# Kernel tuning notes

Measured on AMD Instinct MI355X. Metric: run time of the kernel, lower is better.

## Reference

```python
import jax, jax.numpy as jnp
import numpy as np

E, K, D_IN, D_H, D_OUT, B = 16, 2, 256, 512, 256, 32768


def setup_inputs() -> dict:
    key = jax.random.key(0)
    ks = jax.random.split(key, 7)
    s_in = 1.0 / np.sqrt(D_IN)
    s_h = 1.0 / np.sqrt(D_H)
    return {
        "x": jax.random.normal(ks[0], (B, D_IN), jnp.float32),
        "Wg": jax.random.normal(ks[1], (D_IN, E), jnp.float32) * s_in,
        "bg": jnp.zeros((E,), jnp.float32),
        "W1": jax.random.normal(ks[2], (E, D_IN, D_H), jnp.float32) * s_in,
        "b1": jnp.zeros((E, D_H), jnp.float32),
        "W2": jax.random.normal(ks[3], (E, D_H, D_OUT), jnp.float32) * s_h,
        "b2": jnp.zeros((E, D_OUT), jnp.float32),
    }


def reference(x, Wg, bg, W1, b1, W2, b2):
    # Gating: softmax over experts, top-k, renormalize routing weights.
    probs = jax.nn.softmax(x @ Wg + bg, axis=-1)            # [B, E]
    top_vals, top_idx = jax.lax.top_k(probs, K)              # [B, K]
    w = top_vals / jnp.sum(top_vals, axis=-1, keepdims=True)  # [B, K]

    # Dense per-expert MLP over all tokens (vectorized dispatch equivalent).
    h = jax.nn.relu(jnp.einsum("bi,eih->ebh", x, W1) + b1[:, None, :])  # [E, B, Dh]
    out_e = jnp.einsum("ebh,eho->ebo", h, W2) + b2[:, None, :]          # [E, B, Do]

    # Gather each token's k assigned expert outputs and combine weighted.
    out_be = jnp.transpose(out_e, (1, 0, 2))                  # [B, E, Do]
    sel = jnp.take_along_axis(out_be, top_idx[:, :, None], axis=1)  # [B, K, Do]
    return jnp.sum(w[:, :, None] * sel, axis=1)               # [B, Do]
```

## Files before the change

kernel.cpp:

```cpp
#include <hip/hip_runtime.h>

#define E_ 16
#define DIN 256
#define DH 512
#define DOUT 256
#define BTOK 32768

typedef _Float16 half8 __attribute__((ext_vector_type(8)));
typedef _Float16 half4v __attribute__((ext_vector_type(4)));
typedef float float4v __attribute__((ext_vector_type(4)));

#define OFF_P1      0u
#define OFF_P2      4194304u
#define OFF_XH      8388608u
#define OFF_SCR     25165824u
#define OFF_TIDX    58720256u
#define OFF_TW      58982400u
#define OFF_STOK    59244544u
#define OFF_SW      59506688u
#define OFF_CNT     59768832u
#define OFF_OFFS    59768960u
#define OFF_CUR     59769088u
#define OFF_TMAP    59769216u
#define MLP_GRID    2048

__global__ __launch_bounds__(256) void pack_kernel(const float* __restrict__ W1,
                                                   const float* __restrict__ W2,
                                                   _Float16* __restrict__ p1,
                                                   _Float16* __restrict__ p2,
                                                   int* __restrict__ counts) {
    int tid = threadIdx.x;
    int bid = blockIdx.x * 4 + (tid >> 6);
    int l = tid & 63;
    int quad = l >> 4, l15 = l & 15;
    if (blockIdx.x == 0 && tid < 16) counts[tid] = 0;
    if (bid < 4096) {
        int ht = bid & 31, kt = (bid >> 5) & 7, e = bid >> 8;
        half8 v;
#pragma unroll
        for (int j = 0; j < 8; ++j)
            v[j] = (_Float16)W1[(e * DIN + kt * 32 + quad * 8 + j) * DH + ht * 16 + l15];
        ((half8*)p1)[bid * 64 + l] = v;
    } else {
        int b2i = bid - 4096;
        int ot = b2i & 15, kt = (b2i >> 4) & 15, e = b2i >> 8;
        half8 v;
#pragma unroll
        for (int j = 0; j < 8; ++j)
            v[j] = (_Float16)W2[(e * DH + kt * 32 + quad * 8 + j) * DOUT + ot * 16 + l15];
        ((half8*)p2)[b2i * 64 + l] = v;
    }
}

__global__ __launch_bounds__(256) void gate_kernel(const float* __restrict__ x,
                                                   const float* __restrict__ Wg,
                                                   const float* __restrict__ bg,
                                                   _Float16* __restrict__ xh,
                                                   int* __restrict__ tidx,
                                                   float* __restrict__ tw,
                                                   int* __restrict__ counts) {
    __shared__ float WgS[DIN * E_];
    __shared__ int hcnt[16];
    int tid = threadIdx.x;
    if (tid < 16) hcnt[tid] = 0;
#pragma unroll
    for (int i = 0; i < 4; ++i)
        ((float4v*)WgS)[tid + i * 256] = ((const float4v*)Wg)[tid + i * 256];
    __syncthreads();

    int q = tid & 7, tg = tid >> 3;
    int t0 = blockIdx.x * 64 + tg * 2;

    float acc[2][16];
#pragma unroll
    for (int tt = 0; tt < 2; ++tt)
#pragma unroll
        for (int e = 0; e < 16; ++e) acc[tt][e] = 0.f;

#pragma unroll
    for (int ii = 0; ii < 8; ++ii) {
        int kb = q * 32 + ii * 4;
        float4v xv[2];
#pragma unroll
        for (int tt = 0; tt < 2; ++tt) {
            xv[tt] = *(const float4v*)&x[(t0 + tt) * DIN + kb];
            half4v hv;
#pragma unroll
            for (int j = 0; j < 4; ++j) hv[j] = (_Float16)xv[tt][j];
            *(half4v*)&xh[(t0 + tt) * DIN + kb] = hv;
        }
#pragma unroll
        for (int j = 0; j < 4; ++j) {
            const float4v* wrow = (const float4v*)&WgS[(kb + j) * 16];
            float4v w0 = wrow[0], w1 = wrow[1], w2 = wrow[2], w3 = wrow[3];
#pragma unroll
            for (int tt = 0; tt < 2; ++tt) {
                float xs = xv[tt][j];
#pragma unroll
                for (int c = 0; c < 4; ++c) {
                    acc[tt][0 + c]  += xs * w0[c];
                    acc[tt][4 + c]  += xs * w1[c];
                    acc[tt][8 + c]  += xs * w2[c];
                    acc[tt][12 + c] += xs * w3[c];
                }
            }
        }
    }
#pragma unroll
    for (int tt = 0; tt < 2; ++tt)
#pragma unroll
        for (int e = 0; e < 16; ++e) {
            acc[tt][e] += __shfl_xor(acc[tt][e], 1);
            acc[tt][e] += __shfl_xor(acc[tt][e], 2);
            acc[tt][e] += __shfl_xor(acc[tt][e], 4);
        }
    if (q == 0) {
#pragma unroll
        for (int tt = 0; tt < 2; ++tt) {
            int b = t0 + tt;
            float m1 = -3.4e38f, m2 = -3.4e38f;
            int i1 = 0, i2 = 0;
#pragma unroll
            for (int e = 0; e < 16; ++e) {
                float v = acc[tt][e] + bg[e];
                if (v > m1) { m2 = m1; i2 = i1; m1 = v; i1 = e; }
                else if (v > m2) { m2 = v; i2 = e; }
            }
            float e2 = __expf(m2 - m1);
            float w1 = 1.f / (1.f + e2);
            tidx[b * 2] = i1; tidx[b * 2 + 1] = i2;
            tw[b * 2] = w1;  tw[b * 2 + 1] = e2 * w1;
            atomicAdd(&hcnt[i1], 1);
            atomicAdd(&hcnt[i2], 1);
        }
    }
    __syncthreads();
    if (tid < 16) atomicAdd(&counts[tid], hcnt[tid]);
}

__global__ void scan_kernel(const int* __restrict__ counts, int* __restrict__ offsets,
                            int* __restrict__ cursor, int* __restrict__ tmap) {
    __shared__ int s_off[17];
    int tid = threadIdx.x;
    for (int i = tid; i < MLP_GRID; i += 64) tmap[i] = -1;
    if (tid == 0) {
        int run = 0;
        for (int e = 0; e < 16; ++e) { s_off[e] = run; run += counts[e]; }
        s_off[16] = run;
    }
    __syncthreads();
    if (tid < 16) {
        int e = tid;
        offsets[e] = s_off[e];
        cursor[e] = s_off[e];
        if (e == 0) offsets[16] = s_off[16];
        int nt = (s_off[e + 1] - s_off[e] + 63) >> 6;
        int xc = e & 7;
        int base = (e >= 8) ? ((s_off[e - 7] - s_off[e - 8] + 63) >> 6) : 0;
        for (int t = 0; t < nt; ++t) {
            int s = base + t;
            if (s < 256) tmap[xc + 8 * s] = (e << 16) | t;
        }
    }
}

__global__ __launch_bounds__(256) void scatter_kernel(const int* __restrict__ tidx,
                                                      const float* __restrict__ tw,
                                                      int* __restrict__ cursor,
                                                      int* __restrict__ stok,
                                                      float* __restrict__ sw) {
    __shared__ int lc[16];
    __shared__ int lbase[16];
    int tid = threadIdx.x;
    if (tid < 16) lc[tid] = 0;
    __syncthreads();
    int g = blockIdx.x * 256 + tid;
    int e = tidx[g];
    int rank = atomicAdd(&lc[e], 1);
    __syncthreads();
    if (tid < 16) lbase[tid] = atomicAdd(&cursor[tid], lc[tid]);
    __syncthreads();
    int pos = lbase[e] + rank;
    stok[pos] = g;
    sw[pos] = tw[g];
}

#define XS 0
#define HS 16384
__global__ __launch_bounds__(512, 4) void mlp_kernel(const _Float16* __restrict__ xh,
                                                     const _Float16* __restrict__ p1,
                                                     const _Float16* __restrict__ p2,
                                                     const float* __restrict__ b1,
                                                     const float* __restrict__ b2,
                                                     const int* __restrict__ offsets,
                                                     const int* __restrict__ stok,
                                                     const float* __restrict__ sw,
                                                     const int* __restrict__ tmap,
                                                     _Float16* __restrict__ scr) {
    __shared__ _Float16 S[32768];
    const int tile = tmap[blockIdx.x];
    if (tile < 0) return;
    const int e = tile >> 16;
    const int ts = (tile & 0xffff) * 64;
    const int off = offsets[e];
    const int ne = offsets[e + 1] - off;
    const int rows = min(64, ne - ts);

    const int tid = threadIdx.x;
    const int w = tid >> 6;
    const int l = tid & 63;
    const int l15 = l & 15;
    const int quad = l >> 4;

#pragma unroll
    for (int j = 0; j < 4; ++j) {
        int tokl = w * 8 + j * 2 + (l >> 5);
        int slot = l & 31;
        int g = slot ^ (tokl & 7);
        int r = tokl; if (r >= rows) r = rows - 1;
        int tok = stok[off + ts + r] >> 1;
        half8 v = *(const half8*)&xh[tok * DIN + g * 8];
        *(half8*)&S[XS + tokl * 256 + slot * 8] = v;
    }

    const half8* p1b = (const half8*)p1;
    const half8* p2b = (const half8*)p2;

    float4v acc2[2][4];
#pragma unroll
    for (int n = 0; n < 2; ++n)
#pragma unroll
        for (int mt = 0; mt < 4; ++mt) acc2[n][mt] = (float4v){0.f, 0.f, 0.f, 0.f};

    __syncthreads();

#pragma unroll
    for (int half = 0; half < 2; ++half) {
        float4v acc1[2][4];
#pragma unroll
        for (int mh = 0; mh < 2; ++mh)
#pragma unroll
            for (int nt = 0; nt < 4; ++nt) acc1[mh][nt] = (float4v){0.f, 0.f, 0.f, 0.f};

        half8 awc[2], awn[2];
#pragma unroll
        for (int mh = 0; mh < 2; ++mh)
            awc[mh] = p1b[((e * 8 + 0) * 32 + half * 16 + w * 2 + mh) * 64 + l];

#pragma unroll
        for (int kt = 0; kt < 8; ++kt) {
            int ktn = kt < 7 ? kt + 1 : 7;
#pragma unroll
            for (int mh = 0; mh < 2; ++mh)
                awn[mh] = p1b[((e * 8 + ktn) * 32 + half * 16 + w * 2 + mh) * 64 + l];
            half8 bq[4];
#pragma unroll
            for (int nt = 0; nt < 4; ++nt) {
                int row = nt * 16 + l15;
                int slot = (kt * 4 + quad) ^ (l15 & 7);
                bq[nt] = *(const half8*)&S[XS + row * 256 + slot * 8];
            }
#pragma unroll
            for (int mh = 0; mh < 2; ++mh) {
#pragma unroll
                for (int nt = 0; nt < 4; ++nt)
                    acc1[mh][nt] = __builtin_amdgcn_mfma_f32_16x16x32_f16(awc[mh], bq[nt], acc1[mh][nt], 0, 0, 0);
            }
            awc[0] = awn[0]; awc[1] = awn[1];
        }
#pragma unroll
        for (int mh = 0; mh < 2; ++mh) {
            int colh = (w * 2 + mh) * 16 + quad * 4;
            float4v b1q = *(const float4v*)&b1[e * DH + half * 256 + colh];
            int gq = colh >> 3;
            int go = (quad & 1) * 4;
#pragma unroll
            for (int nt = 0; nt < 4; ++nt) {
                int row = nt * 16 + l15;
                int slot = gq ^ (l15 & 7);
                half4v hv;
#pragma unroll
                for (int r = 0; r < 4; ++r) {
                    float v = acc1[mh][nt][r] + b1q[r];
                    hv[r] = (_Float16)(v > 0.f ? v : 0.f);
                }
                *(half4v*)&S[HS + row * 256 + slot * 8 + go] = hv;
            }
        }
        __syncthreads();

        half8 bwc[2], bwn[2];
#pragma unroll
        for (int n = 0; n < 2; ++n)
            bwc[n] = p2b[((e * 16 + half * 8 + 0) * 16 + w * 2 + n) * 64 + l];

#pragma unroll
        for (int kt2 = 0; kt2 < 8; ++kt2) {
            int ktn = kt2 < 7 ? kt2 + 1 : 7;
#pragma unroll
            for (int n = 0; n < 2; ++n)
                bwn[n] = p2b[((e * 16 + half * 8 + ktn) * 16 + w * 2 + n) * 64 + l];
            half8 ha[4];
#pragma unroll
            for (int mt = 0; mt < 4; ++mt) {
                int row = mt * 16 + l15;
                int slot = (kt2 * 4 + quad) ^ (l15 & 7);
                ha[mt] = *(const half8*)&S[HS + row * 256 + slot * 8];
            }
#pragma unroll
            for (int n = 0; n < 2; ++n) {
#pragma unroll
                for (int mt = 0; mt < 4; ++mt)
                    acc2[n][mt] = __builtin_amdgcn_mfma_f32_16x16x32_f16(bwc[n], ha[mt], acc2[n][mt], 0, 0, 0);
            }
            bwc[0] = bwn[0]; bwc[1] = bwn[1];
        }
        __syncthreads();
    }

#pragma unroll
    for (int n = 0; n < 2; ++n) {
        int col0 = (w * 2 + n) * 16 + quad * 4;
        float4v b2q = *(const float4v*)&b2[e * DOUT + col0];
        int gran = col0 >> 3;
        int go = (quad & 1) * 4;
#pragma unroll
        for (int mt = 0; mt < 4; ++mt) {
            int tok = mt * 16 + l15;
            int rc = tok < rows ? tok : rows - 1;
            float wt = sw[off + ts + rc];
            half4v hv;
#pragma unroll
            for (int r = 0; r < 4; ++r)
                hv[r] = (_Float16)(wt * (acc2[n][mt][r] + b2q[r]));
            int slot = gran ^ (tok & 7);
            *(half4v*)&S[HS + tok * 256 + slot * 8 + go] = hv;
        }
    }
    __syncthreads();
#pragma unroll
    for (int p = 0; p < 4; ++p) {
        int idx = p * 512 + tid;
        int tok = idx >> 5;
        int sl = idx & 31;
        if (tok < rows) {
            int slot = sl ^ (tok & 7);
            half8 v = *(const half8*)&S[HS + tok * 256 + slot * 8];
            int g = stok[off + ts + tok];
            *(half8*)&scr[g * DOUT + sl * 8] = v;
        }
    }
}

__global__ __launch_bounds__(256) void combine_kernel(const _Float16* __restrict__ scr,
                                                      float* __restrict__ out) {
    int wv = threadIdx.x >> 6;
    int l = threadIdx.x & 63;
    int t = blockIdx.x * 4 + wv;
    half4v a = ((const half4v*)(scr + t * 2 * DOUT))[l];
    half4v b = ((const half4v*)(scr + t * 2 * DOUT + DOUT))[l];
    float4v o;
#pragma unroll
    for (int j = 0; j < 4; ++j) o[j] = (float)a[j] + (float)b[j];
    ((float4v*)(out + t * DOUT))[l] = o;
}

extern "C" void kernel_launch(void* const* d_in, const int* in_sizes, int n_in,
                              void* d_out, int out_size, void* d_ws, size_t ws_size,
                              hipStream_t stream) {
    const float* x  = (const float*)d_in[0];
    const float* Wg = (const float*)d_in[1];
    const float* bg = (const float*)d_in[2];
    const float* W1 = (const float*)d_in[3];
    const float* b1 = (const float*)d_in[4];
    const float* W2 = (const float*)d_in[5];
    const float* b2 = (const float*)d_in[6];
    float* out = (float*)d_out;

    char* ws = (char*)d_ws;
    _Float16* p1  = (_Float16*)(ws + OFF_P1);
    _Float16* p2  = (_Float16*)(ws + OFF_P2);
    _Float16* xh  = (_Float16*)(ws + OFF_XH);
    _Float16* scr = (_Float16*)(ws + OFF_SCR);
    int* tidx     = (int*)(ws + OFF_TIDX);
    float* tw     = (float*)(ws + OFF_TW);
    int* stok     = (int*)(ws + OFF_STOK);
    float* swp    = (float*)(ws + OFF_SW);
    int* counts   = (int*)(ws + OFF_CNT);
    int* offsets  = (int*)(ws + OFF_OFFS);
    int* cursor   = (int*)(ws + OFF_CUR);
    int* tmap     = (int*)(ws + OFF_TMAP);

    pack_kernel<<<dim3(2048), dim3(256), 0, stream>>>(W1, W2, p1, p2, counts);
    gate_kernel<<<dim3(512), dim3(256), 0, stream>>>(x, Wg, bg, xh, tidx, tw, counts);
    scan_kernel<<<dim3(1), dim3(64), 0, stream>>>(counts, offsets, cursor, tmap);
    scatter_kernel<<<dim3(256), dim3(256), 0, stream>>>(tidx, tw, cursor, stok, swp);
    mlp_kernel<<<dim3(MLP_GRID), dim3(512), 0, stream>>>(xh, p1, p2, b1, b2, offsets,
                                                         stok, swp, tmap, scr);
    combine_kernel<<<dim3(8192), dim3(256), 0, stream>>>(scr, out);
}
```

Baseline: 200.1 us.

## Merge pack and gate kernels; replace global atomics and scan kernel with per-block histogram

```diff
diff --git a/kernel.cpp b/kernel.cpp
--- a/kernel.cpp
+++ b/kernel.cpp
@@ -14,54 +14,54 @@
 #define OFF_P2      4194304u
 #define OFF_XH      8388608u
 #define OFF_SCR     25165824u
+#define OFF_HIST    25165824u
 #define OFF_TIDX    58720256u
 #define OFF_TW      58982400u
 #define OFF_STOK    59244544u
 #define OFF_SW      59506688u
-#define OFF_CNT     59768832u
 #define OFF_OFFS    59768960u
-#define OFF_CUR     59769088u
 #define OFF_TMAP    59769216u
 #define MLP_GRID    2048
 
-__global__ __launch_bounds__(256) void pack_kernel(const float* __restrict__ W1,
+__global__ __launch_bounds__(256) void prep_kernel(const float* __restrict__ W1,
                                                    const float* __restrict__ W2,
+                                                   const float* __restrict__ x,
+                                                   const float* __restrict__ Wg,
+                                                   const float* __restrict__ bg,
                                                    _Float16* __restrict__ p1,
                                                    _Float16* __restrict__ p2,
-                                                   int* __restrict__ counts) {
-    int tid = threadIdx.x;
-    int bid = blockIdx.x * 4 + (tid >> 6);
-    int l = tid & 63;
-    int quad = l >> 4, l15 = l & 15;
-    if (blockIdx.x == 0 && tid < 16) counts[tid] = 0;
-    if (bid < 4096) {
-        int ht = bid & 31, kt = (bid >> 5) & 7, e = bid >> 8;
-        half8 v;
-#pragma unroll
-        for (int j = 0; j < 8; ++j)
-            v[j] = (_Float16)W1[(e * DIN + kt * 32 + quad * 8 + j) * DH + ht * 16 + l15];
-        ((half8*)p1)[bid * 64 + l] = v;
-    } else {
-        int b2i = bid - 4096;
-        int ot = b2i & 15, kt = (b2i >> 4) & 15, e = b2i >> 8;
-        half8 v;
-#pragma unroll
-        for (int j = 0; j < 8; ++j)
-            v[j] = (_Float16)W2[(e * DH + kt * 32 + quad * 8 + j) * DOUT + ot * 16 + l15];
-        ((half8*)p2)[b2i * 64 + l] = v;
-    }
-}
-
-__global__ __launch_bounds__(256) void gate_kernel(const float* __restrict__ x,
-                                                   const float* __restrict__ Wg,
-                                                   const float* __restrict__ bg,
                                                    _Float16* __restrict__ xh,
                                                    int* __restrict__ tidx,
                                                    float* __restrict__ tw,
-                                                   int* __restrict__ counts) {
+                                                   int* __restrict__ hist) {
     __shared__ float WgS[DIN * E_];
     __shared__ int hcnt[16];
     int tid = threadIdx.x;
+
+    if (blockIdx.x < 2048) {
+        int bid = blockIdx.x * 4 + (tid >> 6);
+        int l = tid & 63;
+        int quad = l >> 4, l15 = l & 15;
+        if (bid < 4096) {
+            int ht = bid & 31, kt = (bid >> 5) & 7, e = bid >> 8;
+            half8 v;
+#pragma unroll
+            for (int j = 0; j < 8; ++j)
+                v[j] = (_Float16)W1[(e * DIN + kt * 32 + quad * 8 + j) * DH + ht * 16 + l15];
+            ((half8*)p1)[bid * 64 + l] = v;
+        } else {
+            int b2i = bid - 4096;
+            int ot = b2i & 15, kt = (b2i >> 4) & 15, e = b2i >> 8;
+            half8 v;
+#pragma unroll
+            for (int j = 0; j < 8; ++j)
+                v[j] = (_Float16)W2[(e * DH + kt * 32 + quad * 8 + j) * DOUT + ot * 16 + l15];
+            ((half8*)p2)[b2i * 64 + l] = v;
+        }
+        return;
+    }
+
+    int gb = blockIdx.x - 2048;
     if (tid < 16) hcnt[tid] = 0;
 #pragma unroll
     for (int i = 0; i < 4; ++i)
@@ -69,7 +69,7 @@
     __syncthreads();
 
     int q = tid & 7, tg = tid >> 3;
-    int t0 = blockIdx.x * 64 + tg * 2;
+    int t0 = gb * 64 + tg * 2;
 
     float acc[2][16];
 #pragma unroll
@@ -135,54 +135,76 @@
         }
     }
     __syncthreads();
-    if (tid < 16) atomicAdd(&counts[tid], hcnt[tid]);
+    if (tid < 16) hist[gb * 16 + tid] = hcnt[tid];
 }
 
-__global__ void scan_kernel(const int* __restrict__ counts, int* __restrict__ offsets,
-                            int* __restrict__ cursor, int* __restrict__ tmap) {
+__global__ __launch_bounds__(256) void scatter_kernel(const int* __restrict__ hist,
+                                                      const int* __restrict__ tidx,
+                                                      const float* __restrict__ tw,
+                                                      int* __restrict__ offsets,
+                                                      int* __restrict__ tmap,
+                                                      int* __restrict__ stok,
+                                                      float* __restrict__ sw) {
+    __shared__ int part_tot[16][17];
+    __shared__ int part_pre[16][17];
     __shared__ int s_off[17];
+    __shared__ int s_base[16];
+    __shared__ int lc[16];
     int tid = threadIdx.x;
-    for (int i = tid; i < MLP_GRID; i += 64) tmap[i] = -1;
+    int b = blockIdx.x;
+    int e = tid & 15, ch = tid >> 4;
+    int gblim = b * 2;
+    int t0 = 0, p0 = 0;
+    for (int i = 0; i < 32; ++i) {
+        int gb = ch * 32 + i;
+        int v = hist[gb * 16 + e];
+        t0 += v;
+        if (gb < gblim) p0 += v;
+    }
+    part_tot[e][ch] = t0;
+    part_pre[e][ch] = p0;
+    if (tid < 16) lc[tid] = 0;
+    __syncthreads();
+    if (tid < 16) {
+        int tot = 0, pre = 0;
+#pragma unroll
+        for (int c = 0; c < 16; ++c) { tot += part_tot[tid][c]; pre += part_pre[tid][c]; }
+        part_tot[tid][16] = tot;
+        part_pre[tid][16] = pre;
+    }
+    __syncthreads();
     if (tid == 0) {
         int run = 0;
-        for (int e = 0; e < 16; ++e) { s_off[e] = run; run += counts[e]; }
+#pragma unroll
+        for (int e2 = 0; e2 < 16; ++e2) { s_off[e2] = run; run += part_tot[e2][16]; }
         s_off[16] = run;
     }
     __syncthreads();
-    if (tid < 16) {
-        int e = tid;
-        offsets[e] = s_off[e];
-        cursor[e] = s_off[e];
-        if (e == 0) offsets[16] = s_off[16];
-        int nt = (s_off[e + 1] - s_off[e] + 63) >> 6;
-        int xc = e & 7;
-        int base = (e >= 8) ? ((s_off[e - 7] - s_off[e - 8] + 63) >> 6) : 0;
-        for (int t = 0; t < nt; ++t) {
-            int s = base + t;
-            if (s < 256) tmap[xc + 8 * s] = (e << 16) | t;
-        }
-    }
-}
-
-__global__ __launch_bounds__(256) void scatter_kernel(const int* __restrict__ tidx,
-                                                      const float* __restrict__ tw,
-                                                      int* __restrict__ cursor,
-                                                      int* __restrict__ stok,
-                                                      float* __restrict__ sw) {
-    __shared__ int lc[16];
-    __shared__ int lbase[16];
-    int tid = threadIdx.x;
-    if (tid < 16) lc[tid] = 0;
-    __syncthreads();
-    int g = blockIdx.x * 256 + tid;
-    int e = tidx[g];
-    int rank = atomicAdd(&lc[e], 1);
-    __syncthreads();
-    if (tid < 16) lbase[tid] = atomicAdd(&cursor[tid], lc[tid]);
-    __syncthreads();
-    int pos = lbase[e] + rank;
+    if (tid < 16) s_base[tid] = s_off[tid] + part_pre[tid][16];
+    __syncthreads();
+
+    int g = b * 256 + tid;
+    int et = tidx[g];
+    int rank = atomicAdd(&lc[et], 1);
+    int pos = s_base[et] + rank;
     stok[pos] = g;
     sw[pos] = tw[g];
+
+    if (b == 0) {
+        if (tid < 17) offsets[tid] = s_off[tid];
+        for (int i = tid; i < MLP_GRID; i += 256) tmap[i] = -1;
+        __syncthreads();
+        if (tid < 16) {
+            int e2 = tid;
+            int nt = (s_off[e2 + 1] - s_off[e2] + 63) >> 6;
+            int xc = e2 & 7;
+            int base = (e2 >= 8) ? ((s_off[e2 - 7] - s_off[e2 - 8] + 63) >> 6) : 0;
+            for (int t = 0; t < nt; ++t) {
+                int s = base + t;
+                if (s < 256) tmap[xc + 8 * s] = (e2 << 16) | t;
+            }
+        }
+    }
 }
 
 #define XS 0
@@ -382,19 +404,18 @@
     _Float16* p2  = (_Float16*)(ws + OFF_P2);
     _Float16* xh  = (_Float16*)(ws + OFF_XH);
     _Float16* scr = (_Float16*)(ws + OFF_SCR);
+    int* hist     = (int*)(ws + OFF_HIST);
     int* tidx     = (int*)(ws + OFF_TIDX);
     float* tw     = (float*)(ws + OFF_TW);
     int* stok     = (int*)(ws + OFF_STOK);
     float* swp    = (float*)(ws + OFF_SW);
-    int* counts   = (int*)(ws + OFF_CNT);
     int* offsets  = (int*)(ws + OFF_OFFS);
-    int* cursor   = (int*)(ws + OFF_CUR);
     int* tmap     = (int*)(ws + OFF_TMAP);
 
-    pack_kernel<<<dim3(2048), dim3(256), 0, stream>>>(W1, W2, p1, p2, counts);
-    gate_kernel<<<dim3(512), dim3(256), 0, stream>>>(x, Wg, bg, xh, tidx, tw, counts);
-    scan_kernel<<<dim3(1), dim3(64), 0, stream>>>(counts, offsets, cursor, tmap);
-    scatter_kernel<<<dim3(256), dim3(256), 0, stream>>>(tidx, tw, cursor, stok, swp);
+    prep_kernel<<<dim3(2560), dim3(256), 0, stream>>>(W1, W2, x, Wg, bg, p1, p2, xh,
+                                                      tidx, tw, hist);
+    scatter_kernel<<<dim3(256), dim3(256), 0, stream>>>(hist, tidx, tw, offsets, tmap,
+                                                        stok, swp);
     mlp_kernel<<<dim3(MLP_GRID), dim3(512), 0, stream>>>(xh, p1, p2, b1, b2, offsets,
                                                          stok, swp, tmap, scr);
     combine_kernel<<<dim3(8192), dim3(256), 0, stream>>>(scr, out);
```

Measured after the change: 209.0 us. +4.4%, slower.
